# Kernel tuning notes

Measured on AMD Instinct MI355X. Metric: run time of the kernel, lower is better.

The kernel has to match this reference:

```python
import jax, jax.numpy as jnp
import numpy as np
from jax import lax

UNITS1 = 256  # lstm_layer (second LSTM, return_sequences=False)
UNITS2 = 256  # hidden_lstm (first LSTM, return_sequences=True)
FEAT = 128


def _glorot(key, shape):
    fan_in, fan_out = shape[0], shape[1]
    lim = jnp.sqrt(6.0 / (fan_in + fan_out))
    return jax.random.uniform(key, shape, jnp.float32, -lim, lim)


def setup_inputs() -> dict:
    key = jax.random.key(0)
    ks = jax.random.split(key, 9)
    B, T = 128, 1024
    x = jax.random.normal(ks[0], (B, T, FEAT), jnp.float32)
    # Layer 1 (hidden_lstm): Keras kernel [in, 4H], recurrent_kernel [H, 4H], bias [4H]
    W1 = _glorot(ks[1], (FEAT, 4 * UNITS2))
    U1 = _glorot(ks[2], (UNITS2, 4 * UNITS2))
    b1 = jnp.zeros((4 * UNITS2,), jnp.float32).at[UNITS2:2 * UNITS2].set(1.0)  # Keras unit_forget_bias
    # Layer 2 (lstm_layer)
    W2 = _glorot(ks[3], (UNITS2, 4 * UNITS1))
    U2 = _glorot(ks[4], (UNITS1, 4 * UNITS1))
    b2 = jnp.zeros((4 * UNITS1,), jnp.float32).at[UNITS1:2 * UNITS1].set(1.0)
    # Output dense: 1 unit, relu
    Wd = _glorot(ks[5], (UNITS1, 1))
    bd = jnp.zeros((1,), jnp.float32)
    return {"x": x, "W1": W1, "U1": U1, "b1": b1,
            "W2": W2, "U2": U2, "b2": b2, "Wd": Wd, "bd": bd}


def _lstm(x, W, U, b, return_sequences):
    # x: [B, T, F]; Keras gate order i, f, c(candidate), o.
    B = x.shape[0]
    H = U.shape[0]
    xW = jnp.einsum('btf,fg->btg', x, W) + b  # precompute input projections: [B, T, 4H]

    def step(carry, xw_t):
        h, c = carry
        g = xw_t + h @ U  # [B, 4H]
        i, f, cand, o = jnp.split(g, 4, axis=-1)
        i = jax.nn.sigmoid(i)
        f = jax.nn.sigmoid(f)
        cand = jnp.tanh(cand)
        o = jax.nn.sigmoid(o)
        c = f * c + i * cand
        h = o * jnp.tanh(c)
        return (h, c), h

    init = (jnp.zeros((B, H), x.dtype), jnp.zeros((B, H), x.dtype))
    (h_last, _), hs = lax.scan(step, init, jnp.swapaxes(xW, 0, 1))  # hs: [T, B, H]
    return jnp.swapaxes(hs, 0, 1) if return_sequences else h_last


def reference(x, W1, U1, b1, W2, U2, b2, Wd, bd):
    h_seq = _lstm(x, W1, U1, b1, return_sequences=True)   # hidden_lstm: [B, T, U2]
    h_last = _lstm(h_seq, W2, U2, b2, return_sequences=False)  # lstm_layer: [B, U1]
    return jax.nn.relu(h_last @ Wd + bd)  # [B, 1]
```

## Files before the change

kernel.cpp:

```cpp
#include <hip/hip_runtime.h>

typedef __bf16 bf16x8 __attribute__((ext_vector_type(8)));
typedef float  f32x4  __attribute__((ext_vector_type(4)));
typedef unsigned short u16;
typedef unsigned int   u32;
typedef unsigned long long u64;

#define NB 128
#define NT 1024
#define NF 128
#define NH 256
#define NG 1024
#define M_ROWS (NB*NT)

__device__ __forceinline__ u16 f2bf(float f) {
  union { float f; u32 u; } c; c.f = f;
  u32 u = c.u;
  return (u16)((u + 0x7fffu + ((u >> 16) & 1u)) >> 16);
}
__device__ __forceinline__ float sigm(float x) { return 1.f / (1.f + __expf(-x)); }
__device__ __forceinline__ float tanh_(float x) { return 1.f - 2.f / (1.f + __expf(2.f * x)); }
__device__ __forceinline__ f32x4 mm(bf16x8 a, bf16x8 b, f32x4 c) {
  return __builtin_amdgcn_mfma_f32_16x16x32_bf16(a, b, c, 0, 0, 0);
}
__device__ __forceinline__ void vm0() { asm volatile("s_waitcnt vmcnt(0)" ::: "memory"); }

__device__ __forceinline__ u32 a_ld32(const u32* p) { return __hip_atomic_load((u32*)p, __ATOMIC_RELAXED, __HIP_MEMORY_SCOPE_AGENT); }
__device__ __forceinline__ u64 a_ld64(const u64* p) { return __hip_atomic_load((u64*)p, __ATOMIC_RELAXED, __HIP_MEMORY_SCOPE_AGENT); }
__device__ __forceinline__ void a_st64(u64* p, u64 v) { __hip_atomic_store(p, v, __ATOMIC_RELAXED, __HIP_MEMORY_SCOPE_AGENT); }
__device__ __forceinline__ void a_add32(u32* p, u32 v) { __hip_atomic_fetch_add(p, v, __ATOMIC_RELAXED, __HIP_MEMORY_SCOPE_AGENT); }

__global__ void prep(u32* __restrict__ flags) {
  if (blockIdx.x == 0 && threadIdx.x < 256) flags[threadIdx.x] = 0;
}

template<bool IS1>
__device__ void scan(const float* __restrict__ U, const float* __restrict__ W,
                     const float* __restrict__ bias, const float* __restrict__ xf,
                     u64* hseq, u64* h2, u32* c1, u32* c2, float* hlast,
                     int g, int j, float (*gl)[16][68])
{
  const int tid = threadIdx.x, lane = tid & 63, w = tid >> 6;
  const int l15 = lane & 15, l16 = lane >> 4;
  constexpr int KIN  = IS1 ? NF : NH;
  constexpr int KTIN = KIN / 32;
  const int colb = w * NH + j * 64;

  bf16x8 wfr[KTIN][4];
#pragma unroll
  for (int kt = 0; kt < KTIN; ++kt) {
    const int k0 = kt * 32 + l16 * 8;
#pragma unroll
    for (int nt = 0; nt < 4; ++nt) {
      const float* wp = W + (long)k0 * NG + colb + nt * 16 + l15;
      union { u16 s[8]; bf16x8 v; } cv;
#pragma unroll
      for (int e = 0; e < 8; ++e) cv.s[e] = f2bf(wp[(long)e * NG]);
      wfr[kt][nt] = cv.v;
    }
  }
  bf16x8 ufr[8][4];
#pragma unroll
  for (int kt = 0; kt < 8; ++kt) {
    const int k0 = kt * 32 + l16 * 8;
#pragma unroll
    for (int nt = 0; nt < 4; ++nt) {
      const float* up = U + (long)k0 * NG + colb + nt * 16 + l15;
      union { u16 s[8]; bf16x8 v; } cv;
#pragma unroll
      for (int e = 0; e < 8; ++e) cv.s[e] = f2bf(up[(long)e * NG]);
      ufr[kt][nt] = cv.v;
    }
  }

  const int prow = tid & 15, ublk = tid >> 4;
  const int b = g * 16 + prow, ucol = j * 64 + ublk * 4;

  float bv[4][4];
#pragma unroll
  for (int gg = 0; gg < 4; ++gg)
#pragma unroll
    for (int q = 0; q < 4; ++q) bv[gg][q] = bias[gg * NH + ucol + q];

  const long abatch = (long)(g * 16 + l15) * NT;

  float cst[4] = {0.f, 0.f, 0.f, 0.f};
  long budget = 2000000;
  bool dead = false;

  for (int t = 0; t < NT; ++t) {
    bf16x8 ax[KTIN];

    if constexpr (IS1) {
      const float* xp0 = xf + (abatch + t) * NF;
      f32x4 xraw[KTIN][2];
#pragma unroll
      for (int kt = 0; kt < KTIN; ++kt) {
        const float* xp = xp0 + kt * 32 + l16 * 8;
        xraw[kt][0] = *reinterpret_cast<const f32x4*>(xp);
        xraw[kt][1] = *reinterpret_cast<const f32x4*>(xp + 4);
      }
#pragma unroll
      for (int kt = 0; kt < KTIN; ++kt) {
        union { u16 s[8]; bf16x8 v; } cv;
#pragma unroll
        for (int e = 0; e < 4; ++e) {
          cv.s[e] = f2bf(xraw[kt][0][e]); cv.s[4 + e] = f2bf(xraw[kt][1][e]);
        }
        ax[kt] = cv.v;
      }
      f32x4 acc[4] = {};
#pragma unroll
      for (int kt = 0; kt < KTIN; ++kt)
#pragma unroll
        for (int nt = 0; nt < 4; ++nt) acc[nt] = mm(ax[kt], wfr[kt][nt], acc[nt]);

      if (t > 0) {
        if (tid == 0 && !dead) {
          const u32 tgt = 16u * (u32)t;
          while (a_ld32(c1) < tgt) {
            __builtin_amdgcn_s_sleep(1);
            if (--budget <= 0) { dead = true; break; }
          }
        }
        __syncthreads();
        asm volatile("" ::: "memory");
        const u64* hb = hseq + (abatch + (t - 1)) * 64;
        u64 hr[8][2];
#pragma unroll
        for (int kt = 0; kt < 8; ++kt) {
          hr[kt][0] = a_ld64(hb + kt * 8 + l16 * 2);
          hr[kt][1] = a_ld64(hb + kt * 8 + l16 * 2 + 1);
        }
#pragma unroll
        for (int kt = 0; kt < 8; ++kt) {
          union { u64 q[2]; bf16x8 v; } cv;
          cv.q[0] = hr[kt][0]; cv.q[1] = hr[kt][1];
#pragma unroll
          for (int nt = 0; nt < 4; ++nt) acc[nt] = mm(cv.v, ufr[kt][nt], acc[nt]);
        }
      }
#pragma unroll
      for (int nt = 0; nt < 4; ++nt)
#pragma unroll
        for (int r = 0; r < 4; ++r)
          gl[w][l16 * 4 + r][nt * 16 + l15] = acc[nt][r];
    } else {
      if (tid == 0 && !dead) {
        const u32 tgtF = 16u * (u32)(t + 1);
        const u32 tgtR = 16u * (u32)t;
        for (;;) {
          u32 v1 = a_ld32(c1);
          u32 v2 = (t > 0) ? a_ld32(c2) : tgtR;
          if (v1 >= tgtF && v2 >= tgtR) break;
          __builtin_amdgcn_s_sleep(1);
          if (--budget <= 0) { dead = true; break; }
        }
      }
      __syncthreads();
      asm volatile("" ::: "memory");

      const u64* xb = hseq + (abatch + t) * 64;
      u64 xr[KTIN][2];
#pragma unroll
      for (int kt = 0; kt < KTIN; ++kt) {
        xr[kt][0] = a_ld64(xb + kt * 8 + l16 * 2);
        xr[kt][1] = a_ld64(xb + kt * 8 + l16 * 2 + 1);
      }
      u64 hr[8][2];
      if (t > 0) {
        const u64* hb = h2 + ((((long)((t + 1) & 1) * 8 + g) * 16) + l15) * 64;
#pragma unroll
        for (int kt = 0; kt < 8; ++kt) {
          hr[kt][0] = a_ld64(hb + kt * 8 + l16 * 2);
          hr[kt][1] = a_ld64(hb + kt * 8 + l16 * 2 + 1);
        }
      }
#pragma unroll
      for (int kt = 0; kt < KTIN; ++kt) {
        union { u64 q[2]; bf16x8 v; } cv;
        cv.q[0] = xr[kt][0]; cv.q[1] = xr[kt][1];
        ax[kt] = cv.v;
      }
      f32x4 acc[4] = {};
#pragma unroll
      for (int kt = 0; kt < KTIN; ++kt)
#pragma unroll
        for (int nt = 0; nt < 4; ++nt) acc[nt] = mm(ax[kt], wfr[kt][nt], acc[nt]);
      if (t > 0) {
#pragma unroll
        for (int kt = 0; kt < 8; ++kt) {
          union { u64 q[2]; bf16x8 v; } cv;
          cv.q[0] = hr[kt][0]; cv.q[1] = hr[kt][1];
#pragma unroll
          for (int nt = 0; nt < 4; ++nt) acc[nt] = mm(cv.v, ufr[kt][nt], acc[nt]);
        }
      }
#pragma unroll
      for (int nt = 0; nt < 4; ++nt)
#pragma unroll
        for (int r = 0; r < 4; ++r)
          gl[w][l16 * 4 + r][nt * 16 + l15] = acc[nt][r];
    }

    __syncthreads();
    f32x4 gi = *reinterpret_cast<const f32x4*>(&gl[0][prow][ublk * 4]);
    f32x4 gf = *reinterpret_cast<const f32x4*>(&gl[1][prow][ublk * 4]);
    f32x4 gc = *reinterpret_cast<const f32x4*>(&gl[2][prow][ublk * 4]);
    f32x4 go = *reinterpret_cast<const f32x4*>(&gl[3][prow][ublk * 4]);
    float hh[4];
#pragma unroll
    for (int q = 0; q < 4; ++q) {
      float iv = sigm(gi[q] + bv[0][q]);
      float fv = sigm(gf[q] + bv[1][q]);
      float cd = tanh_(gc[q] + bv[2][q]);
      float ov = sigm(go[q] + bv[3][q]);
      cst[q] = fv * cst[q] + iv * cd;
      hh[q] = ov * tanh_(cst[q]);
    }
    union { u16 s[4]; u64 q; } hp;
#pragma unroll
    for (int q = 0; q < 4; ++q) hp.s[q] = f2bf(hh[q]);

    if constexpr (IS1) {
      a_st64(hseq + ((long)b * NT + t) * 64 + (ucol >> 2), hp.q);
    } else {
      a_st64(h2 + ((((long)(t & 1) * 8 + g) * 16) + prow) * 64 + (ucol >> 2), hp.q);
      if (t == NT - 1)
        *reinterpret_cast<f32x4*>(hlast + (long)b * NH + ucol) =
            f32x4{hh[0], hh[1], hh[2], hh[3]};
    }
    vm0();
    if (lane == 0) a_add32(IS1 ? c1 : c2, 1u);
  }
}

__global__ __launch_bounds__(256, 1) void lstm_fused(
    const float* __restrict__ x,
    const float* __restrict__ W1, const float* __restrict__ U1, const float* __restrict__ b1,
    const float* __restrict__ W2, const float* __restrict__ U2, const float* __restrict__ b2,
    u64* hseq, u64* h2, u32* flags, float* hlast)
{
  __shared__ __align__(16) float gl[4][16][68];
  const int bid = blockIdx.x;
  const int sb  = bid & 31, g = sb & 7, j = sb >> 3;
  u32* c1 = flags + g * 16;
  u32* c2 = flags + 128 + g * 16;
  if (bid < 32)
    scan<true >(U1, W1, b1, x, hseq, h2, c1, c2, nullptr, g, j, gl);
  else
    scan<false>(U2, W2, b2, nullptr, hseq, h2, c1, c2, hlast, g, j, gl);
}

__global__ void dense_out(const float* __restrict__ hl, const float* __restrict__ Wd,
                          const float* __restrict__ bd, float* __restrict__ out) {
  int b = blockIdx.x, l = threadIdx.x;
  f32x4 h  = *reinterpret_cast<const f32x4*>(hl + (long)b * NH + l * 4);
  f32x4 wv = *reinterpret_cast<const f32x4*>(Wd + l * 4);
  float s = h[0] * wv[0] + h[1] * wv[1] + h[2] * wv[2] + h[3] * wv[3];
#pragma unroll
  for (int off = 32; off > 0; off >>= 1) s += __shfl_down(s, off);
  if (l == 0) out[b] = fmaxf(s + bd[0], 0.f);
}

extern "C" void kernel_launch(void* const* d_in, const int* in_sizes, int n_in,
                              void* d_out, int out_size, void* d_ws, size_t ws_size,
                              hipStream_t stream) {
  const float* x  = (const float*)d_in[0];
  const float* W1 = (const float*)d_in[1];
  const float* U1 = (const float*)d_in[2];
  const float* b1 = (const float*)d_in[3];
  const float* W2 = (const float*)d_in[4];
  const float* U2 = (const float*)d_in[5];
  const float* b2 = (const float*)d_in[6];
  const float* Wd = (const float*)d_in[7];
  const float* bd = (const float*)d_in[8];
  float* out = (float*)d_out;

  char* ws = (char*)d_ws;
  size_t off = 0;
  auto alloc = [&](size_t bytes) -> char* {
    char* p = ws + off;
    off = (off + bytes + 255) & ~(size_t)255;
    return p;
  };
  u64*   hseq  = (u64*)  alloc((size_t)M_ROWS * NH * 2);
  u64*   h2    = (u64*)  alloc((size_t)2 * 8 * 16 * NH * 2);
  float* hlast = (float*)alloc((size_t)NB * NH * 4);
  u32*   flags = (u32*)  alloc(1024);

  if (off > ws_size) {
    hipMemsetAsync(d_out, 0x42, (size_t)out_size * sizeof(float), stream);
    return;
  }

  prep<<<1, 256, 0, stream>>>(flags);
  lstm_fused<<<64, 256, 0, stream>>>(x, W1, U1, b1, W2, U2, b2, hseq, h2, flags, hlast);
  dense_out<<<128, 64, 0, stream>>>(hlast, Wd, bd, out);
}
```

Before: 6.278 ms.

## Replace counter-flag handshakes with sentinel-polled data in LSTM pipeline

Drops the per-step atomic counters, the vmcnt wait before incrementing them, and the single-thread sleep poll followed by a barrier. Each wave now spins directly on the hidden-state data until no word equals an all-ones sentinel. A new prep kernel fills the whole hseq buffer and a 4-deep h2 ring with sentinels, and layer 2 re-arms the next ring slot after each write. This is meant to cut per-timestep handoff latency on the serial recurrence. The costs are a large extra initialisation write, busy polling traffic, and an extra barrier around the shared gate buffer.

```diff
diff --git a/kernel.cpp b/kernel.cpp
--- a/kernel.cpp
+++ b/kernel.cpp
@@ -12,6 +12,7 @@
 #define NH 256
 #define NG 1024
 #define M_ROWS (NB*NT)
+#define SENT (~0ull)
 
 __device__ __forceinline__ u16 f2bf(float f) {
   union { float f; u32 u; } c; c.f = f;
@@ -23,21 +24,20 @@
 __device__ __forceinline__ f32x4 mm(bf16x8 a, bf16x8 b, f32x4 c) {
   return __builtin_amdgcn_mfma_f32_16x16x32_bf16(a, b, c, 0, 0, 0);
 }
-__device__ __forceinline__ void vm0() { asm volatile("s_waitcnt vmcnt(0)" ::: "memory"); }
-
-__device__ __forceinline__ u32 a_ld32(const u32* p) { return __hip_atomic_load((u32*)p, __ATOMIC_RELAXED, __HIP_MEMORY_SCOPE_AGENT); }
+
 __device__ __forceinline__ u64 a_ld64(const u64* p) { return __hip_atomic_load((u64*)p, __ATOMIC_RELAXED, __HIP_MEMORY_SCOPE_AGENT); }
 __device__ __forceinline__ void a_st64(u64* p, u64 v) { __hip_atomic_store(p, v, __ATOMIC_RELAXED, __HIP_MEMORY_SCOPE_AGENT); }
-__device__ __forceinline__ void a_add32(u32* p, u32 v) { __hip_atomic_fetch_add(p, v, __ATOMIC_RELAXED, __HIP_MEMORY_SCOPE_AGENT); }
-
-__global__ void prep(u32* __restrict__ flags) {
-  if (blockIdx.x == 0 && threadIdx.x < 256) flags[threadIdx.x] = 0;
+
+__global__ void prep(u64* __restrict__ hseq, u64* __restrict__ h2) {
+  long i = (long)blockIdx.x * 256 + threadIdx.x;
+  if (i < (long)M_ROWS * 64) a_st64(hseq + i, SENT);
+  if (i < 4L * 8 * 16 * 64)  a_st64(h2 + i, SENT);
 }
 
 template<bool IS1>
 __device__ void scan(const float* __restrict__ U, const float* __restrict__ W,
                      const float* __restrict__ bias, const float* __restrict__ xf,
-                     u64* hseq, u64* h2, u32* c1, u32* c2, float* hlast,
+                     u64* hseq, u64* h2, float* hlast,
                      int g, int j, float (*gl)[16][68])
 {
   const int tid = threadIdx.x, lane = tid & 63, w = tid >> 6;
@@ -72,6 +72,16 @@
       ufr[kt][nt] = cv.v;
     }
   }
+#pragma unroll
+  for (int kt = 0; kt < KTIN; ++kt)
+#pragma unroll
+    for (int nt = 0; nt < 4; ++nt)
+      asm volatile("" : "+v"(wfr[kt][nt]));
+#pragma unroll
+  for (int kt = 0; kt < 8; ++kt)
+#pragma unroll
+    for (int nt = 0; nt < 4; ++nt)
+      asm volatile("" : "+v"(ufr[kt][nt]));
 
   const int prow = tid & 15, ublk = tid >> 4;
   const int b = g * 16 + prow, ucol = j * 64 + ublk * 4;
@@ -85,11 +95,11 @@
   const long abatch = (long)(g * 16 + l15) * NT;
 
   float cst[4] = {0.f, 0.f, 0.f, 0.f};
-  long budget = 2000000;
-  bool dead = false;
+  long budget = 500000;
 
   for (int t = 0; t < NT; ++t) {
     bf16x8 ax[KTIN];
+    f32x4 acc[4] = {};
 
     if constexpr (IS1) {
       const float* xp0 = xf + (abatch + t) * NF;
@@ -109,29 +119,28 @@
         }
         ax[kt] = cv.v;
       }
-      f32x4 acc[4] = {};
 #pragma unroll
       for (int kt = 0; kt < KTIN; ++kt)
 #pragma unroll
         for (int nt = 0; nt < 4; ++nt) acc[nt] = mm(ax[kt], wfr[kt][nt], acc[nt]);
 
       if (t > 0) {
-        if (tid == 0 && !dead) {
-          const u32 tgt = 16u * (u32)t;
-          while (a_ld32(c1) < tgt) {
-            __builtin_amdgcn_s_sleep(1);
-            if (--budget <= 0) { dead = true; break; }
-          }
-        }
-        __syncthreads();
-        asm volatile("" ::: "memory");
         const u64* hb = hseq + (abatch + (t - 1)) * 64;
         u64 hr[8][2];
-#pragma unroll
-        for (int kt = 0; kt < 8; ++kt) {
-          hr[kt][0] = a_ld64(hb + kt * 8 + l16 * 2);
-          hr[kt][1] = a_ld64(hb + kt * 8 + l16 * 2 + 1);
-        }
+        for (;;) {
+          bool ok = true;
+#pragma unroll
+          for (int kt = 0; kt < 8; ++kt) {
+            hr[kt][0] = a_ld64(hb + kt * 8 + l16 * 2);
+            hr[kt][1] = a_ld64(hb + kt * 8 + l16 * 2 + 1);
+          }
+#pragma unroll
+          for (int kt = 0; kt < 8; ++kt)
+            ok = ok && (hr[kt][0] != SENT) && (hr[kt][1] != SENT);
+          if (__all(ok ? 1 : 0)) break;
+          if (--budget <= 0) break;
+        }
+        asm volatile("" ::: "memory");
 #pragma unroll
         for (int kt = 0; kt < 8; ++kt) {
           union { u64 q[2]; bf16x8 v; } cv;
@@ -140,49 +149,40 @@
           for (int nt = 0; nt < 4; ++nt) acc[nt] = mm(cv.v, ufr[kt][nt], acc[nt]);
         }
       }
-#pragma unroll
-      for (int nt = 0; nt < 4; ++nt)
-#pragma unroll
-        for (int r = 0; r < 4; ++r)
-          gl[w][l16 * 4 + r][nt * 16 + l15] = acc[nt][r];
     } else {
-      if (tid == 0 && !dead) {
-        const u32 tgtF = 16u * (u32)(t + 1);
-        const u32 tgtR = 16u * (u32)t;
-        for (;;) {
-          u32 v1 = a_ld32(c1);
-          u32 v2 = (t > 0) ? a_ld32(c2) : tgtR;
-          if (v1 >= tgtF && v2 >= tgtR) break;
-          __builtin_amdgcn_s_sleep(1);
-          if (--budget <= 0) { dead = true; break; }
-        }
-      }
-      __syncthreads();
+      const u64* xb = hseq + (abatch + t) * 64;
+      const u64* hb = h2 + (((long)((t + 3) & 3) * 8 + g) * 16 + l15) * 64;
+      u64 xr[8][2], hr[8][2];
+      for (;;) {
+        bool ok = true;
+#pragma unroll
+        for (int kt = 0; kt < 8; ++kt) {
+          xr[kt][0] = a_ld64(xb + kt * 8 + l16 * 2);
+          xr[kt][1] = a_ld64(xb + kt * 8 + l16 * 2 + 1);
+        }
+#pragma unroll
+        for (int kt = 0; kt < 8; ++kt)
+          ok = ok && (xr[kt][0] != SENT) && (xr[kt][1] != SENT);
+        if (t > 0) {
+#pragma unroll
+          for (int kt = 0; kt < 8; ++kt) {
+            hr[kt][0] = a_ld64(hb + kt * 8 + l16 * 2);
+            hr[kt][1] = a_ld64(hb + kt * 8 + l16 * 2 + 1);
+          }
+#pragma unroll
+          for (int kt = 0; kt < 8; ++kt)
+            ok = ok && (hr[kt][0] != SENT) && (hr[kt][1] != SENT);
+        }
+        if (__all(ok ? 1 : 0)) break;
+        if (--budget <= 0) break;
+      }
       asm volatile("" ::: "memory");
-
-      const u64* xb = hseq + (abatch + t) * 64;
-      u64 xr[KTIN][2];
-#pragma unroll
-      for (int kt = 0; kt < KTIN; ++kt) {
-        xr[kt][0] = a_ld64(xb + kt * 8 + l16 * 2);
-        xr[kt][1] = a_ld64(xb + kt * 8 + l16 * 2 + 1);
-      }
-      u64 hr[8][2];
-      if (t > 0) {
-        const u64* hb = h2 + ((((long)((t + 1) & 1) * 8 + g) * 16) + l15) * 64;
-#pragma unroll
-        for (int kt = 0; kt < 8; ++kt) {
-          hr[kt][0] = a_ld64(hb + kt * 8 + l16 * 2);
-          hr[kt][1] = a_ld64(hb + kt * 8 + l16 * 2 + 1);
-        }
-      }
 #pragma unroll
       for (int kt = 0; kt < KTIN; ++kt) {
         union { u64 q[2]; bf16x8 v; } cv;
         cv.q[0] = xr[kt][0]; cv.q[1] = xr[kt][1];
         ax[kt] = cv.v;
       }
-      f32x4 acc[4] = {};
 #pragma unroll
       for (int kt = 0; kt < KTIN; ++kt)
 #pragma unroll
@@ -196,18 +196,20 @@
           for (int nt = 0; nt < 4; ++nt) acc[nt] = mm(cv.v, ufr[kt][nt], acc[nt]);
         }
       }
-#pragma unroll
-      for (int nt = 0; nt < 4; ++nt)
-#pragma unroll
-        for (int r = 0; r < 4; ++r)
-          gl[w][l16 * 4 + r][nt * 16 + l15] = acc[nt][r];
-    }
-
+    }
+
+#pragma unroll
+    for (int nt = 0; nt < 4; ++nt)
+#pragma unroll
+      for (int r = 0; r < 4; ++r)
+        gl[w][l16 * 4 + r][nt * 16 + l15] = acc[nt][r];
     __syncthreads();
     f32x4 gi = *reinterpret_cast<const f32x4*>(&gl[0][prow][ublk * 4]);
     f32x4 gf = *reinterpret_cast<const f32x4*>(&gl[1][prow][ublk * 4]);
     f32x4 gc = *reinterpret_cast<const f32x4*>(&gl[2][prow][ublk * 4]);
     f32x4 go = *reinterpret_cast<const f32x4*>(&gl[3][prow][ublk * 4]);
+    __syncthreads();
+
     float hh[4];
 #pragma unroll
     for (int q = 0; q < 4; ++q) {
@@ -225,13 +227,12 @@
     if constexpr (IS1) {
       a_st64(hseq + ((long)b * NT + t) * 64 + (ucol >> 2), hp.q);
     } else {
-      a_st64(h2 + ((((long)(t & 1) * 8 + g) * 16) + prow) * 64 + (ucol >> 2), hp.q);
+      a_st64(h2 + (((long)(t & 3) * 8 + g) * 16 + prow) * 64 + (ucol >> 2), hp.q);
+      a_st64(h2 + (((long)((t + 1) & 3) * 8 + g) * 16 + prow) * 64 + (ucol >> 2), SENT);
       if (t == NT - 1)
         *reinterpret_cast<f32x4*>(hlast + (long)b * NH + ucol) =
             f32x4{hh[0], hh[1], hh[2], hh[3]};
     }
-    vm0();
-    if (lane == 0) a_add32(IS1 ? c1 : c2, 1u);
   }
 }
 
@@ -239,17 +240,15 @@
     const float* __restrict__ x,
     const float* __restrict__ W1, const float* __restrict__ U1, const float* __restrict__ b1,
     const float* __restrict__ W2, const float* __restrict__ U2, const float* __restrict__ b2,
-    u64* hseq, u64* h2, u32* flags, float* hlast)
+    u64* hseq, u64* h2, float* hlast)
 {
   __shared__ __align__(16) float gl[4][16][68];
   const int bid = blockIdx.x;
   const int sb  = bid & 31, g = sb & 7, j = sb >> 3;
-  u32* c1 = flags + g * 16;
-  u32* c2 = flags + 128 + g * 16;
   if (bid < 32)
-    scan<true >(U1, W1, b1, x, hseq, h2, c1, c2, nullptr, g, j, gl);
+    scan<true >(U1, W1, b1, x, hseq, h2, nullptr, g, j, gl);
   else
-    scan<false>(U2, W2, b2, nullptr, hseq, h2, c1, c2, hlast, g, j, gl);
+    scan<false>(U2, W2, b2, nullptr, hseq, h2, hlast, g, j, gl);
 }
 
 __global__ void dense_out(const float* __restrict__ hl, const float* __restrict__ Wd,
@@ -285,16 +284,15 @@
     return p;
   };
   u64*   hseq  = (u64*)  alloc((size_t)M_ROWS * NH * 2);
-  u64*   h2    = (u64*)  alloc((size_t)2 * 8 * 16 * NH * 2);
+  u64*   h2    = (u64*)  alloc((size_t)4 * 8 * 16 * NH * 2);
   float* hlast = (float*)alloc((size_t)NB * NH * 4);
-  u32*   flags = (u32*)  alloc(1024);
 
   if (off > ws_size) {
     hipMemsetAsync(d_out, 0x42, (size_t)out_size * sizeof(float), stream);
     return;
   }
 
-  prep<<<1, 256, 0, stream>>>(flags);
-  lstm_fused<<<64, 256, 0, stream>>>(x, W1, U1, b1, W2, U2, b2, hseq, h2, flags, hlast);
+  prep<<<32768, 256, 0, stream>>>(hseq, h2);
+  lstm_fused<<<64, 256, 0, stream>>>(x, W1, U1, b1, W2, U2, b2, hseq, h2, hlast);
   dense_out<<<128, 64, 0, stream>>>(hlast, Wd, bd, out);
 }
```

New measurement: 5.690 ms. 1.1x faster.
